# Kernel tuning notes

Hardware: AMD Instinct MI355X
Metric: run time of the kernel (lower is better)

## Reference

```python
import jax, jax.numpy as jnp
import numpy as np
import math

N_HEADS = 16
KV_HEADS = 4
HEAD_DIM = 128
ROPE_BASE = 1000000.0


def _make_rope(seq_len, dim, base=ROPE_BASE):
    inv_freq = 1.0 / (base ** (np.arange(0, dim, 2, dtype=np.float32) / dim))
    t = np.arange(seq_len, dtype=np.float32)
    freqs = np.outer(t, inv_freq)                     # [S, dim/2]
    emb = np.concatenate([freqs, freqs], axis=-1)     # [S, dim]
    return jnp.asarray(np.cos(emb)), jnp.asarray(np.sin(emb))


def setup_inputs() -> dict:
    key = jax.random.key(0)
    ks = jax.random.split(key, 6)
    B, S, H = 2, 2048, 2048
    kv_dim = KV_HEADS * HEAD_DIM
    s = 1.0 / math.sqrt(H)
    x = jax.random.normal(ks[0], (B, S, H), jnp.float32)
    wq = jax.random.normal(ks[1], (H, H), jnp.float32) * s
    wk = jax.random.normal(ks[2], (kv_dim, H), jnp.float32) * s
    wv = jax.random.normal(ks[3], (kv_dim, H), jnp.float32) * s
    wo = jax.random.normal(ks[4], (H, H), jnp.float32) * s
    bq = jnp.zeros((H,), jnp.float32)
    bk = jnp.zeros((kv_dim,), jnp.float32)
    bv = jnp.zeros((kv_dim,), jnp.float32)
    bo = jnp.zeros((H,), jnp.float32)
    cos, sin = _make_rope(S, HEAD_DIM)
    return {"x": x, "wq": wq, "bq": bq, "wk": wk, "bk": bk,
            "wv": wv, "bv": bv, "wo": wo, "bo": bo, "cos": cos, "sin": sin}


def _rotate_half(t):
    half = t.shape[-1] // 2
    return jnp.concatenate([-t[..., half:], t[..., :half]], axis=-1)


def reference(x, wq, bq, wk, bk, wv, bv, wo, bo, cos, sin):
    B, S, H = x.shape
    hd, nh, kvh = HEAD_DIM, N_HEADS, KV_HEADS
    rep = nh // kvh

    q = (x @ wq.T + bq).reshape(B, S, nh, hd)
    k = (x @ wk.T + bk).reshape(B, S, kvh, hd)
    v = (x @ wv.T + bv).reshape(B, S, kvh, hd)

    # RoPE (rotate-half), cos/sin: [S, hd] -> broadcast over batch and heads
    c = cos[None, :, None, :]
    s_ = sin[None, :, None, :]
    q = q * c + _rotate_half(q) * s_
    k = k * c + _rotate_half(k) * s_

    # GQA: expand KV heads by rep
    k = jnp.repeat(k, rep, axis=2)   # [B, S, nh, hd]
    v = jnp.repeat(v, rep, axis=2)

    q = q.transpose(0, 2, 1, 3)      # [B, nh, S, hd]
    k = k.transpose(0, 2, 1, 3)
    v = v.transpose(0, 2, 1, 3)

    score = jnp.einsum('bhqd,bhkd->bhqk', q, k) / math.sqrt(hd)
    causal = jnp.triu(jnp.full((S, S), -jnp.inf, jnp.float32), k=1)
    score = score + causal
    attn = jax.nn.softmax(score.astype(jnp.float32), axis=-1).astype(q.dtype)

    out = jnp.einsum('bhqk,bhkd->bhqd', attn, v)   # [B, nh, S, hd]
    out = out.transpose(0, 2, 1, 3).reshape(B, S, nh * hd)
    return out @ wo.T + bo
```

## Files before the change

### kernel.cpp

```cpp
#include <hip/hip_runtime.h>

typedef unsigned short u16;
typedef __bf16 bf16x8 __attribute__((ext_vector_type(8)));
typedef float  f32x4  __attribute__((ext_vector_type(4)));

#define SEQ 2048

__device__ __forceinline__ float bf2f(u16 u) {
    union { unsigned int i; float f; } c;
    c.i = ((unsigned int)u) << 16;
    return c.f;
}
__device__ __forceinline__ u16 f2bf(float f) {
    union { float f; unsigned int i; } c;
    c.f = f;
    unsigned int u = c.i;
    u += 0x7FFFu + ((u >> 16) & 1u);
    return (u16)(u >> 16);
}

__device__ __forceinline__ void gl_lds16(const u16* g, u16* l) {
    __builtin_amdgcn_global_load_lds(
        (const __attribute__((address_space(1))) unsigned int*)(g),
        (__attribute__((address_space(3))) unsigned int*)(l), 16, 0, 0);
}

__device__ __forceinline__ void cvt4(const float* s, u16* d) {
    float4 v = *(const float4*)s;
    ushort4 o;
    o.x = f2bf(v.x); o.y = f2bf(v.y); o.z = f2bf(v.z); o.w = f2bf(v.w);
    *(ushort4*)d = o;
}

__global__ void prep(const float* __restrict__ x,
                     const float* __restrict__ wq, const float* __restrict__ wk,
                     const float* __restrict__ wv,
                     const float* __restrict__ bq, const float* __restrict__ bk,
                     const float* __restrict__ bv,
                     u16* __restrict__ xb, u16* __restrict__ wqkvb,
                     float* __restrict__ biasb)
{
    const int E0 = 2097152;
    const int E1 = E0 + 1048576;
    const int E2 = E1 + 262144;
    const int E3 = E2 + 262144;
    const int E4 = E3 + 768;
    int i = blockIdx.x * blockDim.x + threadIdx.x;
    int stride = gridDim.x * blockDim.x;
    for (; i < E4; i += stride) {
        if (i < E0)      cvt4(x  + (size_t)i * 4,        xb    + (size_t)i * 4);
        else if (i < E1) cvt4(wq + (size_t)(i - E0) * 4, wqkvb + (size_t)(i - E0) * 4);
        else if (i < E2) cvt4(wk + (size_t)(i - E1) * 4, wqkvb + 4194304 + (size_t)(i - E1) * 4);
        else if (i < E3) cvt4(wv + (size_t)(i - E2) * 4, wqkvb + 5242880 + (size_t)(i - E2) * 4);
        else {
            int j = i - E3;
            const float* src = (j < 512) ? (bq + j * 4)
                             : (j < 640) ? (bk + (j - 512) * 4)
                                         : (bv + (j - 640) * 4);
            *(float4*)&biasb[j * 4] = *(const float4*)src;
        }
    }
}

__global__ void cvt_f32_bf16(const float* __restrict__ in, u16* __restrict__ out, int n4) {
    int i = blockIdx.x * blockDim.x + threadIdx.x;
    int stride = gridDim.x * blockDim.x;
    for (; i < n4; i += stride) cvt4(in + (size_t)i * 4, out + (size_t)i * 4);
}

template<int MODE>
__global__ __launch_bounds__(256) void gemm_bt(
    const u16* __restrict__ A, const u16* __restrict__ B,
    const float* __restrict__ bias, float* __restrict__ C,
    u16* __restrict__ qb, u16* __restrict__ kb, u16* __restrict__ vt,
    int M, int N, int K)
{
    __shared__ __align__(16) u16 lA[128 * 32];
    __shared__ __align__(16) u16 lB[128 * 32];
    const int tid   = threadIdx.x;
    const int lane  = tid & 63;
    const int wave  = tid >> 6;
    const int waveM = (wave >> 1) * 64;
    const int waveN = (wave & 1) * 64;
    const int bm = blockIdx.x * 128;
    const int bn = blockIdx.y * 128;
    const int lrow = lane & 15;
    const int koff = (lane >> 4) * 8;

    f32x4 acc[4][4] = {};

    for (int k0 = 0; k0 < K; k0 += 32) {
        __syncthreads();
#pragma unroll
        for (int p = 0; p < 2; ++p) {
            int idx = p * 256 + tid;
            int row = idx >> 2;
            int ch  = idx & 3;
            gl_lds16(&A[(size_t)(bm + row) * K + k0 + ch * 8], &lA[(p * 256 + wave * 64) * 8]);
            gl_lds16(&B[(size_t)(bn + row) * K + k0 + ch * 8], &lB[(p * 256 + wave * 64) * 8]);
        }
        __syncthreads();

        bf16x8 af[4], bfr[4];
#pragma unroll
        for (int i = 0; i < 4; ++i)
            af[i] = *(const bf16x8*)&lA[(waveM + i * 16 + lrow) * 32 + koff];
#pragma unroll
        for (int j = 0; j < 4; ++j)
            bfr[j] = *(const bf16x8*)&lB[(waveN + j * 16 + lrow) * 32 + koff];
#pragma unroll
        for (int i = 0; i < 4; ++i)
#pragma unroll
            for (int j = 0; j < 4; ++j)
                acc[i][j] = __builtin_amdgcn_mfma_f32_16x16x32_bf16(
                    af[i], bfr[j], acc[i][j], 0, 0, 0);
    }

    const int r4 = (lane >> 4) * 4;
    const int cn = lane & 15;
#pragma unroll
    for (int i = 0; i < 4; ++i) {
#pragma unroll
        for (int j = 0; j < 4; ++j) {
            int row0 = bm + waveM + i * 16 + r4;
            int col  = bn + waveN + j * 16 + cn;
            float bc = bias[col];
#pragma unroll
            for (int r = 0; r < 4; ++r) {
                float val = acc[i][j][r] + bc;
                if (MODE == 0) {
                    C[(size_t)(row0 + r) * N + col] = val;
                } else {
                    int row = row0 + r;
                    int b = row >> 11;
                    int s = row & 2047;
                    int d = col & 127;
                    u16 o = f2bf(val);
                    if (col < 2048) {
                        int h = col >> 7;
                        qb[(((size_t)(b * 16 + h) * SEQ) + s) * 128 + d] = o;
                    } else if (col < 2560) {
                        int h = (col - 2048) >> 7;
                        kb[(((size_t)(b * 4 + h) * SEQ) + s) * 128 + d] = o;
                    } else {
                        int h = (col - 2560) >> 7;
                        vt[(((size_t)(b * 4 + h) * 128) + d) * SEQ + s] = o;
                    }
                }
            }
        }
    }
}

__global__ void rope_inplace(u16* __restrict__ qb, u16* __restrict__ kb,
                             const float* __restrict__ cosb, const float* __restrict__ sinb)
{
    const int n = (65536 + 16384) * 64;
    int i = blockIdx.x * blockDim.x + threadIdx.x;
    if (i >= n) return;
    int d0  = i & 63;
    int row = i >> 6;
    u16* base;
    if (row < 65536) base = qb + (size_t)row * 128;
    else             base = kb + (size_t)(row - 65536) * 128;
    int s = row & (SEQ - 1);
    float c  = cosb[s * 128 + d0];
    float sn = sinb[s * 128 + d0];
    float a0 = bf2f(base[d0]);
    float a1 = bf2f(base[d0 + 64]);
    base[d0]      = f2bf(a0 * c - a1 * sn);
    base[d0 + 64] = f2bf(a1 * c + a0 * sn);
}

__global__ __launch_bounds__(256, 2) void attn_mfma(
    const u16* __restrict__ qb, const u16* __restrict__ kb,
    const u16* __restrict__ vt, u16* __restrict__ ob)
{
    __shared__ __align__(16) u16 Ks[2][4][64][32];
    __shared__ __align__(16) u16 Vts[2][2][128][32];
    __shared__ __align__(16) u16 Ph[4][16][64];

    const int id   = blockIdx.x;
    const int s8   = id & 7;
    const int n    = id >> 3;
    const int pair = n & 15;
    const int h_lo = n >> 4;
    const int b    = s8 >> 2;
    const int kvh  = s8 & 3;
    const int h    = kvh * 4 + h_lo;
    const int qA   = pair, qB = 31 - pair;

    const int tid  = threadIdx.x;
    const int lane = tid & 63;
    const int w    = tid >> 6;
    const int c16  = lane & 15;
    const int quad = lane >> 4;
    const float qscale = 0.08838834764831845f * 1.4426950408889634f;

    const u16* kbase  = kb + ((size_t)(b * 4 + kvh) * SEQ) * 128;
    const u16* vtbase = vt + ((size_t)(b * 4 + kvh) * 128) * SEQ;

    bf16x8 qfA[4], qfB[4];
    {
        const u16* qpA = qb + (((size_t)(b * 16 + h)) * SEQ + qA * 64 + w * 16 + c16) * 128;
        const u16* qpB = qb + (((size_t)(b * 16 + h)) * SEQ + qB * 64 + w * 16 + c16) * 128;
#pragma unroll
        for (int kk = 0; kk < 4; ++kk) {
            bf16x8 ta = *(const bf16x8*)(qpA + kk * 32 + quad * 8);
            bf16x8 tb = *(const bf16x8*)(qpB + kk * 32 + quad * 8);
#pragma unroll
            for (int e = 0; e < 8; ++e) {
                ta[e] = (__bf16)((float)ta[e] * qscale);
                tb[e] = (__bf16)((float)tb[e] * qscale);
            }
            qfA[kk] = ta; qfB[kk] = tb;
        }
    }

    int ksrc[4], vsrc[4];
#pragma unroll
    for (int it = 0; it < 4; ++it) {
        int o  = (it * 4 + w) * 1024 + lane * 16;
        int kk = o >> 12;
        int r  = (o >> 6) & 63;
        int c  = (o >> 4) & 3;
        ksrc[it] = r * 128 + kk * 32 + c * 8;
        int p2 = o >> 13;
        int d  = (o >> 6) & 127;
        vsrc[it] = d * SEQ + p2 * 32 + c * 8;
    }

    const int nB = qB + 1;
    const int rowLA = qA * 64 + w * 16 + quad * 4;
    const int rowLB = qB * 64 + w * 16 + quad * 4;

    f32x4 oA[8] = {}, oB[8] = {};
    float lA[4] = {}, lB[4] = {};

    u16* KsF  = &Ks[0][0][0][0];
    u16* VtsF = &Vts[0][0][0][0];

#pragma unroll
    for (int it = 0; it < 4; ++it) {
        gl_lds16(kbase  + ksrc[it], KsF  + (it * 4 + w) * 512);
        gl_lds16(vtbase + vsrc[it], VtsF + (it * 4 + w) * 512);
    }
    __syncthreads();

    for (int kt = 0; kt < nB; ++kt) {
        const int cur = kt & 1;

        if (kt + 1 < nB) {
            const u16* kg = kbase  + (size_t)(kt + 1) * (64 * 128);
            const u16* vg = vtbase + (kt + 1) * 64;
            u16* kd = KsF  + ((kt + 1) & 1) * (4 * 64 * 32);
            u16* vd = VtsF + ((kt + 1) & 1) * (2 * 128 * 32);
#pragma unroll
            for (int it = 0; it < 4; ++it) {
                gl_lds16(kg + ksrc[it], kd + (it * 4 + w) * 512);
                gl_lds16(vg + vsrc[it], vd + (it * 4 + w) * 512);
            }
        }

        const bool doA = kt <= qA;

        f32x4 sA[4] = {}, sB[4] = {};
        if (doA) {
#pragma unroll
            for (int kk = 0; kk < 4; ++kk)
#pragma unroll
                for (int j = 0; j < 4; ++j) {
                    bf16x8 kf = *(const bf16x8*)&Ks[cur][kk][j * 16 + c16][quad * 8];
                    sA[j] = __builtin_amdgcn_mfma_f32_16x16x32_bf16(qfA[kk], kf, sA[j], 0, 0, 0);
                    sB[j] = __builtin_amdgcn_mfma_f32_16x16x32_bf16(qfB[kk], kf, sB[j], 0, 0, 0);
                }
        } else {
#pragma unroll
            for (int kk = 0; kk < 4; ++kk)
#pragma unroll
                for (int j = 0; j < 4; ++j) {
                    bf16x8 kf = *(const bf16x8*)&Ks[cur][kk][j * 16 + c16][quad * 8];
                    sB[j] = __builtin_amdgcn_mfma_f32_16x16x32_bf16(qfB[kk], kf, sB[j], 0, 0, 0);
                }
        }

        if (doA && kt == qA) {
#pragma unroll
            for (int j = 0; j < 4; ++j)
#pragma unroll
                for (int rr = 0; rr < 4; ++rr)
                    if (kt * 64 + j * 16 + c16 > rowLA + rr) sA[j][rr] = -1e30f;
        }
        if (kt == qB) {
#pragma unroll
            for (int j = 0; j < 4; ++j)
#pragma unroll
                for (int rr = 0; rr < 4; ++rr)
                    if (kt * 64 + j * 16 + c16 > rowLB + rr) sB[j][rr] = -1e30f;
        }

        bf16x8 paA[2], paB[2];
        if (doA) {
#pragma unroll
            for (int jj = 0; jj < 4; ++jj)
#pragma unroll
                for (int rr = 0; rr < 4; ++rr) {
                    float p = __builtin_amdgcn_exp2f(sA[jj][rr]);
                    lA[rr] += p;
                    int row = quad * 4 + rr;
                    *(__bf16*)&Ph[w][row][(((jj * 2 + (c16 >> 3)) + row) & 7) * 8 + (c16 & 7)] = (__bf16)p;
                }
#pragma unroll
            for (int k2 = 0; k2 < 2; ++k2)
                paA[k2] = *(const bf16x8*)&Ph[w][c16][(((k2 * 4 + quad) + c16) & 7) * 8];
        }
#pragma unroll
        for (int jj = 0; jj < 4; ++jj)
#pragma unroll
            for (int rr = 0; rr < 4; ++rr) {
                float p = __builtin_amdgcn_exp2f(sB[jj][rr]);
                lB[rr] += p;
                int row = quad * 4 + rr;
                *(__bf16*)&Ph[w][row][(((jj * 2 + (c16 >> 3)) + row) & 7) * 8 + (c16 & 7)] = (__bf16)p;
            }
#pragma unroll
        for (int k2 = 0; k2 < 2; ++k2)
            paB[k2] = *(const bf16x8*)&Ph[w][c16][(((k2 * 4 + quad) + c16) & 7) * 8];

        if (doA) {
#pragma unroll
            for (int k2 = 0; k2 < 2; ++k2)
#pragma unroll
                for (int nt = 0; nt < 8; ++nt) {
                    bf16x8 vf = *(const bf16x8*)&Vts[cur][k2][nt * 16 + c16][quad * 8];
                    oA[nt] = __builtin_amdgcn_mfma_f32_16x16x32_bf16(paA[k2], vf, oA[nt], 0, 0, 0);
                    oB[nt] = __builtin_amdgcn_mfma_f32_16x16x32_bf16(paB[k2], vf, oB[nt], 0, 0, 0);
                }
        } else {
#pragma unroll
            for (int k2 = 0; k2 < 2; ++k2)
#pragma unroll
                for (int nt = 0; nt < 8; ++nt) {
                    bf16x8 vf = *(const bf16x8*)&Vts[cur][k2][nt * 16 + c16][quad * 8];
                    oB[nt] = __builtin_amdgcn_mfma_f32_16x16x32_bf16(paB[k2], vf, oB[nt], 0, 0, 0);
                }
        }

        __syncthreads();
    }

    float liA[4], liB[4];
#pragma unroll
    for (int rr = 0; rr < 4; ++rr) {
        float la = lA[rr], lb = lB[rr];
        la += __shfl_xor(la, 1); lb += __shfl_xor(lb, 1);
        la += __shfl_xor(la, 2); lb += __shfl_xor(lb, 2);
        la += __shfl_xor(la, 4); lb += __shfl_xor(lb, 4);
        la += __shfl_xor(la, 8); lb += __shfl_xor(lb, 8);
        liA[rr] = 1.0f / la;     liB[rr] = 1.0f / lb;
    }
    const size_t rowGA = (size_t)b * SEQ + rowLA;
    const size_t rowGB = (size_t)b * SEQ + rowLB;
#pragma unroll
    for (int nt = 0; nt < 8; ++nt)
#pragma unroll
        for (int rr = 0; rr < 4; ++rr) {
            ob[(rowGA + rr) * 2048 + h * 128 + nt * 16 + c16] = f2bf(oA[nt][rr] * liA[rr]);
            ob[(rowGB + rr) * 2048 + h * 128 + nt * 16 + c16] = f2bf(oB[nt][rr] * liB[rr]);
        }
}

extern "C" void kernel_launch(void* const* d_in, const int* in_sizes, int n_in,
                              void* d_out, int out_size, void* d_ws, size_t ws_size,
                              hipStream_t stream) {
    const float* x    = (const float*)d_in[0];
    const float* wq   = (const float*)d_in[1];
    const float* bq   = (const float*)d_in[2];
    const float* wk   = (const float*)d_in[3];
    const float* bk   = (const float*)d_in[4];
    const float* wv   = (const float*)d_in[5];
    const float* bv   = (const float*)d_in[6];
    const float* wo   = (const float*)d_in[7];
    const float* bo   = (const float*)d_in[8];
    const float* cosb = (const float*)d_in[9];
    const float* sinb = (const float*)d_in[10];
    float* out = (float*)d_out;

    char* ws = (char*)d_ws;
    const size_t OFF_WQKV = 0;
    const size_t OFF_BIAS = 12582912;
    const size_t OFF_QB   = 12599296;
    const size_t OFF_KB   = 29376512;
    const size_t OFF_VT   = 33570816;
    const size_t OFF_XB   = 37765120;

    u16*   wqkvb = (u16*)(ws + OFF_WQKV);
    u16*   wob   = (u16*)(ws + OFF_WQKV);
    float* biasb = (float*)(ws + OFF_BIAS);
    u16*   qb2   = (u16*)(ws + OFF_QB);
    u16*   kb2   = (u16*)(ws + OFF_KB);
    u16*   vt2   = (u16*)(ws + OFF_VT);
    u16*   xb    = (u16*)(ws + OFF_XB);
    u16*   attnb = (u16*)(ws + OFF_XB);

    prep<<<4096, 256, 0, stream>>>(x, wq, wk, wv, bq, bk, bv, xb, wqkvb, biasb);

    gemm_bt<1><<<dim3(32, 24), 256, 0, stream>>>(xb, wqkvb, biasb, nullptr,
                                                 qb2, kb2, vt2, 4096, 3072, 2048);

    cvt_f32_bf16<<<4096, 256, 0, stream>>>(wo, wob, 1048576);

    rope_inplace<<<((65536 + 16384) * 64) / 256, 256, 0, stream>>>(qb2, kb2, cosb, sinb);

    attn_mfma<<<512, 256, 0, stream>>>(qb2, kb2, vt2, attnb);

    gemm_bt<0><<<dim3(32, 16), 256, 0, stream>>>(attnb, wob, bo, out,
                                                 nullptr, nullptr, nullptr, 4096, 2048, 2048);
}
```

Before: 347.3 us.

## Assign each query tile to a pair of waves instead of splitting rows across all four

```diff
diff --git a/kernel.cpp b/kernel.cpp
--- a/kernel.cpp
+++ b/kernel.cpp
@@ -195,25 +195,24 @@
     const int w    = tid >> 6;
     const int c16  = lane & 15;
     const int quad = lane >> 4;
+    const int T    = w >> 1;
+    const int sub  = w & 1;
+    const int qT   = T ? qB : qA;
     const float qscale = 0.08838834764831845f * 1.4426950408889634f;
 
     const u16* kbase  = kb + ((size_t)(b * 4 + kvh) * SEQ) * 128;
-    const u16* vtbase = vt + ((size_t)(b * 4 + kvh) * 128) * SEQ;
-
-    bf16x8 qfA[4], qfB[4];
-    {
-        const u16* qpA = qb + (((size_t)(b * 16 + h)) * SEQ + qA * 64 + w * 16 + c16) * 128;
-        const u16* qpB = qb + (((size_t)(b * 16 + h)) * SEQ + qB * 64 + w * 16 + c16) * 128;
+    const u16* vtbase = vt + ((size_t)(b * 4 + kvh) * 128) * 128 * (SEQ / 128);
+
+    bf16x8 qf[2][4];
+#pragma unroll
+    for (int s = 0; s < 2; ++s) {
+        const u16* qp = qb + (((size_t)(b * 16 + h)) * SEQ + qT * 64 + sub * 32 + s * 16 + c16) * 128;
 #pragma unroll
         for (int kk = 0; kk < 4; ++kk) {
-            bf16x8 ta = *(const bf16x8*)(qpA + kk * 32 + quad * 8);
-            bf16x8 tb = *(const bf16x8*)(qpB + kk * 32 + quad * 8);
-#pragma unroll
-            for (int e = 0; e < 8; ++e) {
-                ta[e] = (__bf16)((float)ta[e] * qscale);
-                tb[e] = (__bf16)((float)tb[e] * qscale);
-            }
-            qfA[kk] = ta; qfB[kk] = tb;
+            bf16x8 t = *(const bf16x8*)(qp + kk * 32 + quad * 8);
+#pragma unroll
+            for (int e = 0; e < 8; ++e) t[e] = (__bf16)((float)t[e] * qscale);
+            qf[s][kk] = t;
         }
     }
 
@@ -231,11 +230,10 @@
     }
 
     const int nB = qB + 1;
-    const int rowLA = qA * 64 + w * 16 + quad * 4;
-    const int rowLB = qB * 64 + w * 16 + quad * 4;
-
-    f32x4 oA[8] = {}, oB[8] = {};
-    float lA[4] = {}, lB[4] = {};
+    const int rowL0 = qT * 64 + sub * 32 + quad * 4;
+
+    f32x4 o[2][8] = {};
+    float l[2][4] = {};
 
     u16* KsF  = &Ks[0][0][0][0];
     u16* VtsF = &Vts[0][0][0][0];
@@ -262,112 +260,76 @@
             }
         }
 
-        const bool doA = kt <= qA;
-
-        f32x4 sA[4] = {}, sB[4] = {};
-        if (doA) {
+        if (T == 1 || kt <= qA) {
+            f32x4 sS[2][4] = {};
 #pragma unroll
             for (int kk = 0; kk < 4; ++kk)
 #pragma unroll
                 for (int j = 0; j < 4; ++j) {
                     bf16x8 kf = *(const bf16x8*)&Ks[cur][kk][j * 16 + c16][quad * 8];
-                    sA[j] = __builtin_amdgcn_mfma_f32_16x16x32_bf16(qfA[kk], kf, sA[j], 0, 0, 0);
-                    sB[j] = __builtin_amdgcn_mfma_f32_16x16x32_bf16(qfB[kk], kf, sB[j], 0, 0, 0);
+                    sS[0][j] = __builtin_amdgcn_mfma_f32_16x16x32_bf16(qf[0][kk], kf, sS[0][j], 0, 0, 0);
+                    sS[1][j] = __builtin_amdgcn_mfma_f32_16x16x32_bf16(qf[1][kk], kf, sS[1][j], 0, 0, 0);
                 }
-        } else {
-#pragma unroll
-            for (int kk = 0; kk < 4; ++kk)
-#pragma unroll
-                for (int j = 0; j < 4; ++j) {
-                    bf16x8 kf = *(const bf16x8*)&Ks[cur][kk][j * 16 + c16][quad * 8];
-                    sB[j] = __builtin_amdgcn_mfma_f32_16x16x32_bf16(qfB[kk], kf, sB[j], 0, 0, 0);
-                }
-        }
-
-        if (doA && kt == qA) {
-#pragma unroll
-            for (int j = 0; j < 4; ++j)
-#pragma unroll
-                for (int rr = 0; rr < 4; ++rr)
-                    if (kt * 64 + j * 16 + c16 > rowLA + rr) sA[j][rr] = -1e30f;
-        }
-        if (kt == qB) {
-#pragma unroll
-            for (int j = 0; j < 4; ++j)
-#pragma unroll
-                for (int rr = 0; rr < 4; ++rr)
-                    if (kt * 64 + j * 16 + c16 > rowLB + rr) sB[j][rr] = -1e30f;
-        }
-
-        bf16x8 paA[2], paB[2];
-        if (doA) {
-#pragma unroll
-            for (int jj = 0; jj < 4; ++jj)
-#pragma unroll
-                for (int rr = 0; rr < 4; ++rr) {
-                    float p = __builtin_amdgcn_exp2f(sA[jj][rr]);
-                    lA[rr] += p;
-                    int row = quad * 4 + rr;
-                    *(__bf16*)&Ph[w][row][(((jj * 2 + (c16 >> 3)) + row) & 7) * 8 + (c16 & 7)] = (__bf16)p;
-                }
-#pragma unroll
-            for (int k2 = 0; k2 < 2; ++k2)
-                paA[k2] = *(const bf16x8*)&Ph[w][c16][(((k2 * 4 + quad) + c16) & 7) * 8];
-        }
-#pragma unroll
-        for (int jj = 0; jj < 4; ++jj)
-#pragma unroll
-            for (int rr = 0; rr < 4; ++rr) {
-                float p = __builtin_amdgcn_exp2f(sB[jj][rr]);
-                lB[rr] += p;
-                int row = quad * 4 + rr;
-                *(__bf16*)&Ph[w][row][(((jj * 2 + (c16 >> 3)) + row) & 7) * 8 + (c16 & 7)] = (__bf16)p;
+
+            if (kt == qT) {
+#pragma unroll
+                for (int s = 0; s < 2; ++s)
+#pragma unroll
+                    for (int j = 0; j < 4; ++j)
+#pragma unroll
+                        for (int rr = 0; rr < 4; ++rr)
+                            if (kt * 64 + j * 16 + c16 > rowL0 + s * 16 + rr) sS[s][j][rr] = -1e30f;
             }
-#pragma unroll
-        for (int k2 = 0; k2 < 2; ++k2)
-            paB[k2] = *(const bf16x8*)&Ph[w][c16][(((k2 * 4 + quad) + c16) & 7) * 8];
-
-        if (doA) {
+
+            bf16x8 pa[2][2];
+#pragma unroll
+            for (int s = 0; s < 2; ++s) {
+#pragma unroll
+                for (int jj = 0; jj < 4; ++jj)
+#pragma unroll
+                    for (int rr = 0; rr < 4; ++rr) {
+                        float p = __builtin_amdgcn_exp2f(sS[s][jj][rr]);
+                        l[s][rr] += p;
+                        int row = quad * 4 + rr;
+                        *(__bf16*)&Ph[w][row][(((jj * 2 + (c16 >> 3)) + row) & 7) * 8 + (c16 & 7)] = (__bf16)p;
+                    }
+#pragma unroll
+                for (int k2 = 0; k2 < 2; ++k2)
+                    pa[s][k2] = *(const bf16x8*)&Ph[w][c16][(((k2 * 4 + quad) + c16) & 7) * 8];
+            }
+
 #pragma unroll
             for (int k2 = 0; k2 < 2; ++k2)
 #pragma unroll
                 for (int nt = 0; nt < 8; ++nt) {
                     bf16x8 vf = *(const bf16x8*)&Vts[cur][k2][nt * 16 + c16][quad * 8];
-                    oA[nt] = __builtin_amdgcn_mfma_f32_16x16x32_bf16(paA[k2], vf, oA[nt], 0, 0, 0);
-                    oB[nt] = __builtin_amdgcn_mfma_f32_16x16x32_bf16(paB[k2], vf, oB[nt], 0, 0, 0);
+                    o[0][nt] = __builtin_amdgcn_mfma_f32_16x16x32_bf16(pa[0][k2], vf, o[0][nt], 0, 0, 0);
+                    o[1][nt] = __builtin_amdgcn_mfma_f32_16x16x32_bf16(pa[1][k2], vf, o[1][nt], 0, 0, 0);
                 }
-        } else {
-#pragma unroll
-            for (int k2 = 0; k2 < 2; ++k2)
-#pragma unroll
-                for (int nt = 0; nt < 8; ++nt) {
-                    bf16x8 vf = *(const bf16x8*)&Vts[cur][k2][nt * 16 + c16][quad * 8];
-                    oB[nt] = __builtin_amdgcn_mfma_f32_16x16x32_bf16(paB[k2], vf, oB[nt], 0, 0, 0);
-                }
         }
 
         __syncthreads();
     }
 
-    float liA[4], liB[4];
-#pragma unroll
-    for (int rr = 0; rr < 4; ++rr) {
-        float la = lA[rr], lb = lB[rr];
-        la += __shfl_xor(la, 1); lb += __shfl_xor(lb, 1);
-        la += __shfl_xor(la, 2); lb += __shfl_xor(lb, 2);
-        la += __shfl_xor(la, 4); lb += __shfl_xor(lb, 4);
-        la += __shfl_xor(la, 8); lb += __shfl_xor(lb, 8);
-        liA[rr] = 1.0f / la;     liB[rr] = 1.0f / lb;
-    }
-    const size_t rowGA = (size_t)b * SEQ + rowLA;
-    const size_t rowGB = (size_t)b * SEQ + rowLB;
-#pragma unroll
-    for (int nt = 0; nt < 8; ++nt)
+#pragma unroll
+    for (int s = 0; s < 2; ++s) {
+        float li[4];
 #pragma unroll
         for (int rr = 0; rr < 4; ++rr) {
-            ob[(rowGA + rr) * 2048 + h * 128 + nt * 16 + c16] = f2bf(oA[nt][rr] * liA[rr]);
-            ob[(rowGB + rr) * 2048 + h * 128 + nt * 16 + c16] = f2bf(oB[nt][rr] * liB[rr]);
-        }
+            float la = l[s][rr];
+            la += __shfl_xor(la, 1);
+            la += __shfl_xor(la, 2);
+            la += __shfl_xor(la, 4);
+            la += __shfl_xor(la, 8);
+            li[rr] = 1.0f / la;
+        }
+        const size_t rowG = (size_t)b * SEQ + rowL0 + s * 16;
+#pragma unroll
+        for (int nt = 0; nt < 8; ++nt)
+#pragma unroll
+            for (int rr = 0; rr < 4; ++rr)
+                ob[(rowG + rr) * 2048 + h * 128 + nt * 16 + c16] = f2bf(o[s][nt][rr] * li[rr]);
+    }
 }
 
 extern "C" void kernel_launch(void* const* d_in, const int* in_sizes, int n_in,
```

Measured after the change: 347.2 us. Within noise of the previous version (-0.0%).
